# Kernel optimization log

Measured on AMD Instinct MI355X. Metric: run time of the kernel, lower is better.

## Reference

```python
import jax, jax.numpy as jnp
import numpy as np

N_ITER = 3


def squash(v):
    # v: [..., out_C]; scale by ||v||^2/(1+||v||^2) and normalize by ||v||
    sq = jnp.sum(v * v, axis=-1, keepdims=True)
    return (sq / (1.0 + sq)) * v / jnp.sqrt(sq)


def setup_inputs() -> dict:
    key = jax.random.key(0)
    k1, k2 = jax.random.split(key)
    B, n_nodes, n_caps, in_C, out_C = 64, 2048, 32, 16, 32
    x = jax.random.normal(k1, (B, n_nodes, in_C), dtype=jnp.float32)
    route_weights = 0.1 * jax.random.normal(k2, (n_nodes, n_caps, in_C, out_C), dtype=jnp.float32)
    return {"x": x, "route_weights": route_weights}


def reference(x, route_weights):
    # priors: [B, n_nodes, n_caps, out_C]
    priors = jnp.einsum('bni,nkio->bnko', x, route_weights)
    logits = jnp.zeros_like(priors)
    outputs = None
    for i in range(N_ITER):
        probs = jax.nn.softmax(logits, axis=2)            # over n_caps
        s = jnp.sum(probs * priors, axis=1, keepdims=True)  # [B,1,n_caps,out_C]
        outputs = squash(s)
        if i != N_ITER - 1:
            delta = jnp.sum(priors * outputs, axis=-1, keepdims=True)
            logits = logits + delta
    return outputs
```

## Files before the change

### kernel.cpp

```cpp
#include <hip/hip_runtime.h>
#include <math.h>


#define BATCH 64
#define NN    2048
#define NK    32
#define NI    16
#define NO    32

#define PNB   16
#define NSETS (NN / PNB)
#define XT_JS 528

typedef __bf16 bf16x8 __attribute__((ext_vector_type(8)));
typedef float  f32x16 __attribute__((ext_vector_type(16)));

__device__ __forceinline__ unsigned short f2bf(float f) {
    unsigned int x = __float_as_uint(f);
    unsigned int lsb = (x >> 16) & 1u;
    x += 0x7fffu + lsb;
    return (unsigned short)(x >> 16);
}
__device__ __forceinline__ float bflo(unsigned int u) { return __uint_as_float(u << 16); }
__device__ __forceinline__ float bfhi(unsigned int u) { return __uint_as_float(u & 0xffff0000u); }

__global__ __launch_bounds__(256) void wqt_kernel(const float* __restrict__ Wg,
                                                  unsigned short* __restrict__ wq) {
    const int w    = threadIdx.x >> 6;
    const int lane = threadIdx.x & 63;
    const int task = blockIdx.x * 4 + w;
    const int o  = lane & 31;
    const int ih = lane >> 5;
    const float* src = Wg + (size_t)task * (NI * NO);
    unsigned short d[8];
#pragma unroll
    for (int j = 0; j < 8; ++j)
        d[j] = f2bf(src[(ih * 8 + j) * NO + o]);
    *(uint4*)(wq + (size_t)task * (NO * NI) + o * NI + ih * 8) = *(uint4*)d;
}

template <int PASS>
__global__ __launch_bounds__(1024) void fused_pass(
    const float* __restrict__ xg,
    const unsigned short* __restrict__ wq,
    const float* __restrict__ outv,
    float* __restrict__ logits0,
    float* __restrict__ part)
{
    __shared__ unsigned short xt_lds[PNB * XT_JS];
    __shared__ float delta_lds[2][32 * 33];

    const int tid  = threadIdx.x;
    const int w    = tid >> 6;
    const int lane = tid & 63;
    const int l5   = lane & 31;
    const int h5   = lane >> 5;
    const int set  = blockIdx.x;
    const int hb   = blockIdx.y;
    const int k0   = 2 * w, k1 = 2 * w + 1;
    const int gb5  = hb * 32 + l5;
    const int sb   = tid >> 5;
    const int sk   = tid & 31;
    const int nbase = set * PNB;

#pragma unroll
    for (int rr = 0; rr < 2; ++rr) {
        const int id  = tid + rr * 1024;
        const int bl  = id >> 6;
        const int rem = id & 63;
        const int j   = rem >> 2;
        const int i4  = rem & 3;
        float4 v = *(const float4*)(xg + ((size_t)(hb * 32 + bl) * NN + (nbase + j)) * NI + i4 * 4);
        ushort4 o4;
        o4.x = f2bf(v.x); o4.y = f2bf(v.y); o4.z = f2bf(v.z); o4.w = f2bf(v.w);
        *(ushort4*)(xt_lds + j * XT_JS + bl * 16 + i4 * 4) = o4;
    }
    __syncthreads();

    unsigned orp0[8], orp1[8];
    if constexpr (PASS >= 1) {
#pragma unroll
        for (int q = 0; q < 8; ++q) {
            const int oA = ((2*q) & 3) + 8 * ((2*q) >> 2) + 4 * h5;
            const int oB = ((2*q+1) & 3) + 8 * ((2*q+1) >> 2) + 4 * h5;
            float a0 = outv[(k0 * NO + oA) * BATCH + gb5];
            float b0 = outv[(k0 * NO + oB) * BATCH + gb5];
            float a1 = outv[(k1 * NO + oA) * BATCH + gb5];
            float b1 = outv[(k1 * NO + oB) * BATCH + gb5];
            orp0[q] = (unsigned)f2bf(a0) | ((unsigned)f2bf(b0) << 16);
            orp1[q] = (unsigned)f2bf(a1) | ((unsigned)f2bf(b1) << 16);
        }
    }

    float sa0[16], sa1[16];
#pragma unroll
    for (int r = 0; r < 16; ++r) { sa0[r] = 0.f; sa1[r] = 0.f; }

    bf16x8 b0N, b1N;
    float gN = 0.f;
    {
        const int n = nbase;
        b0N = *(const bf16x8*)(wq + (size_t)n * (NK * NO * NI) + k0 * (NO * NI) + l5 * NI + h5 * 8);
        b1N = *(const bf16x8*)(wq + (size_t)n * (NK * NO * NI) + k1 * (NO * NI) + l5 * NI + h5 * 8);
        if constexpr (PASS == 2)
            gN = logits0[(size_t)n * (BATCH * NK) + hb * 1024 + tid];
    }

    int buf = 0;
    for (int j = 0; j < PNB; ++j) {
        const int n = nbase + j;
        const bf16x8 b0C = b0N, b1C = b1N;
        const float gC = gN;
        if (j < PNB - 1) {
            const int n2 = n + 1;
            b0N = *(const bf16x8*)(wq + (size_t)n2 * (NK * NO * NI) + k0 * (NO * NI) + l5 * NI + h5 * 8);
            b1N = *(const bf16x8*)(wq + (size_t)n2 * (NK * NO * NI) + k1 * (NO * NI) + l5 * NI + h5 * 8);
            if constexpr (PASS == 2)
                gN = logits0[(size_t)n2 * (BATCH * NK) + hb * 1024 + tid];
        }
        const bf16x8 aC = *(const bf16x8*)(xt_lds + j * XT_JS + l5 * 16 + h5 * 8);

        f32x16 c0, c1;
#pragma unroll
        for (int r = 0; r < 16; ++r) { c0[r] = 0.f; c1[r] = 0.f; }
        c0 = __builtin_amdgcn_mfma_f32_32x32x16_bf16(b0C, aC, c0, 0, 0, 0);
        c1 = __builtin_amdgcn_mfma_f32_32x32x16_bf16(b1C, aC, c1, 0, 0, 0);

        if constexpr (PASS == 0) {
#pragma unroll
            for (int r = 0; r < 16; ++r) { sa0[r] += c0[r]; sa1[r] += c1[r]; }
        } else {
            float d0 = 0.f, d1 = 0.f;
#pragma unroll
            for (int r = 0; r < 16; ++r) {
                const unsigned u0 = orp0[r >> 1], u1 = orp1[r >> 1];
                const float o0 = (r & 1) ? bfhi(u0) : bflo(u0);
                const float o1 = (r & 1) ? bfhi(u1) : bflo(u1);
                d0 = fmaf(c0[r], o0, d0);
                d1 = fmaf(c1[r], o1, d1);
            }
            d0 += __shfl_xor(d0, 32);
            d1 += __shfl_xor(d1, 32);

            delta_lds[buf][l5 * 33 + (h5 ? k1 : k0)] = h5 ? d1 : d0;
            __syncthreads();

            float l = delta_lds[buf][sb * 33 + sk];
            if constexpr (PASS == 1)
                logits0[(size_t)n * (BATCH * NK) + hb * 1024 + tid] = l;
            else
                l += gC;
            float e = __expf(l);
            float s = e;
#pragma unroll
            for (int mask = 1; mask < 32; mask <<= 1)
                s += __shfl_xor(s, mask);
            delta_lds[buf][sb * 33 + sk] = e / s;
            __syncthreads();

            const float p0 = delta_lds[buf][l5 * 33 + k0];
            const float p1 = delta_lds[buf][l5 * 33 + k1];
#pragma unroll
            for (int r = 0; r < 16; ++r) {
                sa0[r] = fmaf(p0, c0[r], sa0[r]);
                sa1[r] = fmaf(p1, c1[r], sa1[r]);
            }
            buf ^= 1;
        }
    }

    const float scale = (PASS == 0) ? (1.f / NK) : 1.f;
    float* pb = part + ((size_t)(hb * NSETS + set) << 15);
#pragma unroll
    for (int r = 0; r < 16; ++r) {
        const int o = (r & 3) + 8 * (r >> 2) + 4 * h5;
        pb[(k0 * NO + o) * 32 + l5] = sa0[r] * scale;
        pb[(k1 * NO + o) * 32 + l5] = sa1[r] * scale;
    }
}

template <int FINAL>
__global__ __launch_bounds__(1024) void reduce_squash3(
    const float* __restrict__ part,
    float* __restrict__ outv,
    float* __restrict__ outp)
{
    __shared__ float s_lds[32 * 33];
    __shared__ float cf_lds[32];
    const int k  = blockIdx.x;
    const int hb = blockIdx.y;
    const int t  = threadIdx.x;
    const int o  = t >> 5;
    const int b  = t & 31;

    const float* src = part + ((size_t)hb * NSETS << 15) + (k << 10) + (o << 5) + b;
    float v0 = 0.f, v1 = 0.f, v2 = 0.f, v3 = 0.f;
#pragma unroll 4
    for (int s = 0; s < NSETS; s += 4) {
        v0 += src[(size_t)(s + 0) << 15];
        v1 += src[(size_t)(s + 1) << 15];
        v2 += src[(size_t)(s + 2) << 15];
        v3 += src[(size_t)(s + 3) << 15];
    }
    const float v = (v0 + v1) + (v2 + v3);
    s_lds[o * 33 + b] = v;
    __syncthreads();
    if (t < 32) {
        float sq = 0.f;
#pragma unroll
        for (int oo = 0; oo < 32; ++oo) { const float x = s_lds[oo * 33 + t]; sq = fmaf(x, x, sq); }
        cf_lds[t] = sq / ((1.f + sq) * sqrtf(sq));
    }
    __syncthreads();
    if (FINAL) {
        const int bq = t >> 5, oq = t & 31;
        outp[(size_t)(hb * 32 + bq) * 1024 + k * 32 + oq] = s_lds[oq * 33 + bq] * cf_lds[bq];
    } else {
        outv[k * 2048 + o * 64 + hb * 32 + b] = v * cf_lds[b];
    }
}


#define LBB 32
#define LNCHUNK 8
#define LNBLK (NN / LNCHUNK)
#define LTHREADS 512
#define WK_STRIDE 516

template <int PASS>
__global__ __launch_bounds__(LTHREADS, 1) void legacy_pass(
    const float* __restrict__ xg, const float* __restrict__ Wg,
    const float* __restrict__ outvL, float* __restrict__ logits,
    float* __restrict__ partial)
{
    __shared__ float w_lds[NK * WK_STRIDE];
    __shared__ float x_lds[LBB][NI + 1];
    __shared__ float delta_lds[LBB][NK + 1];
    const int t = threadIdx.x, nb = blockIdx.x, bg = blockIdx.y;
    const int b0 = bg * LBB;
    const int k = t >> 4, bq = t & 15, bl0 = bq * 2, bl1 = bq * 2 + 1;
    float acc0[NO], acc1[NO];
#pragma unroll
    for (int o = 0; o < NO; ++o) { acc0[o] = 0.f; acc1[o] = 0.f; }
    float outr0[NO], outr1[NO];
    if constexpr (PASS >= 1) {
        const float4* o0 = (const float4*)&outvL[((b0 + bl0) * NK + k) * NO];
        const float4* o1 = (const float4*)&outvL[((b0 + bl1) * NK + k) * NO];
#pragma unroll
        for (int q = 0; q < NO / 4; ++q) {
            float4 a = o0[q]; float4 b = o1[q];
            outr0[4*q+0]=a.x; outr0[4*q+1]=a.y; outr0[4*q+2]=a.z; outr0[4*q+3]=a.w;
            outr1[4*q+0]=b.x; outr1[4*q+1]=b.y; outr1[4*q+2]=b.z; outr1[4*q+3]=b.w;
        }
    }
    for (int j = 0; j < LNCHUNK; ++j) {
        const int n = nb * LNCHUNK + j;
        __syncthreads();
        {
            const float4* src = (const float4*)(Wg + (size_t)n * (NK * NI * NO));
#pragma unroll
            for (int r = 0; r < (NK * NI * NO / 4) / LTHREADS; ++r) {
                int idx4 = t + r * LTHREADS;
                float4 v = src[idx4];
                int e = idx4 * 4, kk = e >> 9, rem = e & 511;
                *(float4*)&w_lds[kk * WK_STRIDE + rem] = v;
            }
        }
        { int bl = t >> 4, i = t & 15;
          x_lds[bl][i] = xg[((size_t)(b0 + bl) * NN + n) * NI + i]; }
        __syncthreads();
        if constexpr (PASS == 0) {
#pragma unroll
            for (int i = 0; i < NI; ++i) {
                float xa = x_lds[bl0][i], xb = x_lds[bl1][i];
                const float* wrow = &w_lds[k * WK_STRIDE + i * NO];
#pragma unroll
                for (int o = 0; o < NO; ++o) {
                    float w = wrow[o];
                    acc0[o] = fmaf(xa, w, acc0[o]);
                    acc1[o] = fmaf(xb, w, acc1[o]);
                }
            }
        } else {
            float pr0[NO], pr1[NO];
#pragma unroll
            for (int o = 0; o < NO; ++o) { pr0[o] = 0.f; pr1[o] = 0.f; }
#pragma unroll
            for (int i = 0; i < NI; ++i) {
                float xa = x_lds[bl0][i], xb = x_lds[bl1][i];
                const float* wrow = &w_lds[k * WK_STRIDE + i * NO];
#pragma unroll
                for (int o = 0; o < NO; ++o) {
                    float w = wrow[o];
                    pr0[o] = fmaf(xa, w, pr0[o]);
                    pr1[o] = fmaf(xb, w, pr1[o]);
                }
            }
            float d0 = 0.f, d1 = 0.f;
#pragma unroll
            for (int o = 0; o < NO; ++o) {
                d0 = fmaf(pr0[o], outr0[o], d0);
                d1 = fmaf(pr1[o], outr1[o], d1);
            }
            float l0 = d0, l1 = d1;
            const size_t li0 = ((size_t)(b0 + bl0) * NN + n) * NK + k;
            const size_t li1 = ((size_t)(b0 + bl1) * NN + n) * NK + k;
            if constexpr (PASS == 2) { l0 += logits[li0]; l1 += logits[li1]; }
            else { logits[li0] = d0; logits[li1] = d1; }
            delta_lds[bl0][k] = l0; delta_lds[bl1][k] = l1;
            __syncthreads();
            float m0 = -1e30f, m1 = -1e30f;
#pragma unroll
            for (int kk = 0; kk < NK; ++kk) {
                m0 = fmaxf(m0, delta_lds[bl0][kk]);
                m1 = fmaxf(m1, delta_lds[bl1][kk]);
            }
            float s0 = 0.f, s1 = 0.f;
#pragma unroll
            for (int kk = 0; kk < NK; ++kk) {
                s0 += __expf(delta_lds[bl0][kk] - m0);
                s1 += __expf(delta_lds[bl1][kk] - m1);
            }
            float p0 = __expf(l0 - m0) / s0;
            float p1 = __expf(l1 - m1) / s1;
#pragma unroll
            for (int o = 0; o < NO; ++o) {
                acc0[o] = fmaf(p0, pr0[o], acc0[o]);
                acc1[o] = fmaf(p1, pr1[o], acc1[o]);
            }
        }
    }
    const float scale = (PASS == 0) ? (1.f / NK) : 1.f;
    float4* p0 = (float4*)&partial[(((size_t)nb * BATCH + (b0 + bl0)) * NK + k) * NO];
    float4* p1 = (float4*)&partial[(((size_t)nb * BATCH + (b0 + bl1)) * NK + k) * NO];
#pragma unroll
    for (int q = 0; q < NO / 4; ++q) {
        float4 v0, v1;
        v0.x = acc0[4*q+0]*scale; v0.y = acc0[4*q+1]*scale;
        v0.z = acc0[4*q+2]*scale; v0.w = acc0[4*q+3]*scale;
        v1.x = acc1[4*q+0]*scale; v1.y = acc1[4*q+1]*scale;
        v1.z = acc1[4*q+2]*scale; v1.w = acc1[4*q+3]*scale;
        p0[q] = v0; p1[q] = v1;
    }
}

__global__ __launch_bounds__(256) void legacy_reduce(
    const float* __restrict__ partial, float* __restrict__ outf)
{
    const int tid = blockIdx.x * 256 + threadIdx.x;
    float v = 0.f;
    for (int nb = 0; nb < LNBLK; ++nb)
        v += partial[(size_t)nb * (BATCH * NK * NO) + tid];
    float sq = v * v;
#pragma unroll
    for (int off = 1; off < 32; off <<= 1) sq += __shfl_xor(sq, off);
    float coef = sq / ((1.f + sq) * sqrtf(sq));
    outf[tid] = v * coef;
}


extern "C" void kernel_launch(void* const* d_in, const int* in_sizes, int n_in,
                              void* d_out, int out_size, void* d_ws, size_t ws_size,
                              hipStream_t stream)
{
    const float* xg = (const float*)d_in[0];
    const float* Wg = (const float*)d_in[1];
    float* outp = (float*)d_out;
    char* ws = (char*)d_ws;

    const size_t SZ_WQ     = (size_t)NN * NK * NO * NI * 2;
    const size_t SZ_PART   = (size_t)256 * 32768 * 4;
    const size_t SZ_LOGITS = (size_t)NN * BATCH * NK * 4;
    const size_t SZ_OUTV   = (size_t)NK * NO * BATCH * 4;
    const size_t NEED = SZ_WQ + SZ_PART + SZ_LOGITS + SZ_OUTV;

    if (ws_size >= NEED) {
        unsigned short* wq = (unsigned short*)ws;
        float* part    = (float*)(ws + SZ_WQ);
        float* logits0 = (float*)(ws + SZ_WQ + SZ_PART);
        float* outv    = (float*)(ws + SZ_WQ + SZ_PART + SZ_LOGITS);

        wqt_kernel<<<16384, 256, 0, stream>>>(Wg, wq);

        dim3 pg(NSETS, 2);
        dim3 rg(NK, 2);
        fused_pass<0><<<pg, 1024, 0, stream>>>(xg, wq, nullptr, nullptr, part);
        reduce_squash3<0><<<rg, 1024, 0, stream>>>(part, outv, nullptr);
        fused_pass<1><<<pg, 1024, 0, stream>>>(xg, wq, outv, logits0, part);
        reduce_squash3<0><<<rg, 1024, 0, stream>>>(part, outv, nullptr);
        fused_pass<2><<<pg, 1024, 0, stream>>>(xg, wq, outv, logits0, part);
        reduce_squash3<1><<<rg, 1024, 0, stream>>>(part, nullptr, outp);
    } else {
        float* partial = (float*)ws;
        float* logits = (float*)(ws + (size_t)LNBLK * BATCH * NK * NO * 4);
        float* outvL = (float*)(ws + (size_t)LNBLK * BATCH * NK * NO * 4 + (size_t)BATCH * NN * NK * 4);
        dim3 grid(LNBLK, BATCH / LBB);
        const int rblocks = BATCH * NK * NO / 256;
        legacy_pass<0><<<grid, LTHREADS, 0, stream>>>(xg, Wg, nullptr, logits, partial);
        legacy_reduce<<<rblocks, 256, 0, stream>>>(partial, outvL);
        legacy_pass<1><<<grid, LTHREADS, 0, stream>>>(xg, Wg, outvL, logits, partial);
        legacy_reduce<<<rblocks, 256, 0, stream>>>(partial, outvL);
        legacy_pass<2><<<grid, LTHREADS, 0, stream>>>(xg, Wg, outvL, logits, partial);
        legacy_reduce<<<rblocks, 256, 0, stream>>>(partial, outp);
    }
}
```

Before: 334.0 us.

## Halve node sets per block and split reduction into chunked two-stage with fused squash

Cuts nodes per block from 16 to 8, which doubles the number of fused_pass blocks, and adds an occupancy hint to launch_bounds. The single 64-block reduction is split into a 4-way chunked stage1 reduction. The squash of the routing outputs is recomputed inside each fused_pass block from the partial sums, and a separate final kernel produces the output. The aim is to raise parallelism in both the main pass and the reduction, which previously had very few blocks. The cost is twice the partial-sum traffic, redundant squash work in every block, and one extra launch.

```diff
diff --git a/kernel.cpp b/kernel.cpp
--- a/kernel.cpp
+++ b/kernel.cpp
@@ -8,8 +8,9 @@
 #define NI    16
 #define NO    32
 
-#define PNB   16
+#define PNB   8
 #define NSETS (NN / PNB)
+#define NCH   4
 #define XT_JS 528
 
 typedef __bf16 bf16x8 __attribute__((ext_vector_type(8)));
@@ -40,10 +41,10 @@
 }
 
 template <int PASS>
-__global__ __launch_bounds__(1024) void fused_pass(
+__global__ __launch_bounds__(1024, 8) void fused_pass(
     const float* __restrict__ xg,
     const unsigned short* __restrict__ wq,
-    const float* __restrict__ outv,
+    const float* __restrict__ vpart,
     float* __restrict__ logits0,
     float* __restrict__ part)
 {
@@ -63,11 +64,9 @@
     const int sk   = tid & 31;
     const int nbase = set * PNB;
 
-#pragma unroll
-    for (int rr = 0; rr < 2; ++rr) {
-        const int id  = tid + rr * 1024;
-        const int bl  = id >> 6;
-        const int rem = id & 63;
+    {
+        const int bl  = tid >> 5;
+        const int rem = tid & 31;
         const int j   = rem >> 2;
         const int i4  = rem & 3;
         float4 v = *(const float4*)(xg + ((size_t)(hb * 32 + bl) * NN + (nbase + j)) * NI + i4 * 4);
@@ -79,16 +78,29 @@
 
     unsigned orp0[8], orp1[8];
     if constexpr (PASS >= 1) {
+        float v0[16], v1[16];
+        float sq0 = 0.f, sq1 = 0.f;
+#pragma unroll
+        for (int r = 0; r < 16; ++r) {
+            const int o = (r & 3) + 8 * (r >> 2) + 4 * h5;
+            float a = 0.f, b = 0.f;
+#pragma unroll
+            for (int c = 0; c < NCH; ++c) {
+                a += vpart[(((size_t)c * NK + k0) * NO + o) * BATCH + gb5];
+                b += vpart[(((size_t)c * NK + k1) * NO + o) * BATCH + gb5];
+            }
+            v0[r] = a; v1[r] = b;
+            sq0 = fmaf(a, a, sq0);
+            sq1 = fmaf(b, b, sq1);
+        }
+        sq0 += __shfl_xor(sq0, 32);
+        sq1 += __shfl_xor(sq1, 32);
+        const float cf0 = sq0 / ((1.f + sq0) * sqrtf(sq0));
+        const float cf1 = sq1 / ((1.f + sq1) * sqrtf(sq1));
 #pragma unroll
         for (int q = 0; q < 8; ++q) {
-            const int oA = ((2*q) & 3) + 8 * ((2*q) >> 2) + 4 * h5;
-            const int oB = ((2*q+1) & 3) + 8 * ((2*q+1) >> 2) + 4 * h5;
-            float a0 = outv[(k0 * NO + oA) * BATCH + gb5];
-            float b0 = outv[(k0 * NO + oB) * BATCH + gb5];
-            float a1 = outv[(k1 * NO + oA) * BATCH + gb5];
-            float b1 = outv[(k1 * NO + oB) * BATCH + gb5];
-            orp0[q] = (unsigned)f2bf(a0) | ((unsigned)f2bf(b0) << 16);
-            orp1[q] = (unsigned)f2bf(a1) | ((unsigned)f2bf(b1) << 16);
+            orp0[q] = (unsigned)f2bf(v0[2 * q] * cf0) | ((unsigned)f2bf(v0[2 * q + 1] * cf0) << 16);
+            orp1[q] = (unsigned)f2bf(v1[2 * q] * cf1) | ((unsigned)f2bf(v1[2 * q + 1] * cf1) << 16);
         }
     }
 
@@ -179,10 +191,32 @@
     }
 }
 
-template <int FINAL>
-__global__ __launch_bounds__(1024) void reduce_squash3(
+__global__ __launch_bounds__(1024) void reduce_stage1(
     const float* __restrict__ part,
-    float* __restrict__ outv,
+    float* __restrict__ vpart)
+{
+    const int k  = blockIdx.x;
+    const int hb = blockIdx.y;
+    const int c  = blockIdx.z;
+    const int t  = threadIdx.x;
+    const int o  = t >> 5;
+    const int b  = t & 31;
+
+    const float* src = part + ((size_t)(hb * NSETS + c * (NSETS / NCH)) << 15)
+                            + (k << 10) + (o << 5) + b;
+    float v0 = 0.f, v1 = 0.f, v2 = 0.f, v3 = 0.f;
+#pragma unroll 4
+    for (int s = 0; s < NSETS / NCH; s += 4) {
+        v0 += src[(size_t)(s + 0) << 15];
+        v1 += src[(size_t)(s + 1) << 15];
+        v2 += src[(size_t)(s + 2) << 15];
+        v3 += src[(size_t)(s + 3) << 15];
+    }
+    vpart[(((size_t)c * NK + k) * NO + o) * BATCH + hb * 32 + b] = (v0 + v1) + (v2 + v3);
+}
+
+__global__ __launch_bounds__(1024) void reduce_final(
+    const float* __restrict__ vpart,
     float* __restrict__ outp)
 {
     __shared__ float s_lds[32 * 33];
@@ -193,16 +227,10 @@
     const int o  = t >> 5;
     const int b  = t & 31;
 
-    const float* src = part + ((size_t)hb * NSETS << 15) + (k << 10) + (o << 5) + b;
-    float v0 = 0.f, v1 = 0.f, v2 = 0.f, v3 = 0.f;
-#pragma unroll 4
-    for (int s = 0; s < NSETS; s += 4) {
-        v0 += src[(size_t)(s + 0) << 15];
-        v1 += src[(size_t)(s + 1) << 15];
-        v2 += src[(size_t)(s + 2) << 15];
-        v3 += src[(size_t)(s + 3) << 15];
-    }
-    const float v = (v0 + v1) + (v2 + v3);
+    float v = 0.f;
+#pragma unroll
+    for (int c = 0; c < NCH; ++c)
+        v += vpart[(((size_t)c * NK + k) * NO + o) * BATCH + hb * 32 + b];
     s_lds[o * 33 + b] = v;
     __syncthreads();
     if (t < 32) {
@@ -212,12 +240,8 @@
         cf_lds[t] = sq / ((1.f + sq) * sqrtf(sq));
     }
     __syncthreads();
-    if (FINAL) {
-        const int bq = t >> 5, oq = t & 31;
-        outp[(size_t)(hb * 32 + bq) * 1024 + k * 32 + oq] = s_lds[oq * 33 + bq] * cf_lds[bq];
-    } else {
-        outv[k * 2048 + o * 64 + hb * 32 + b] = v * cf_lds[b];
-    }
+    const int bq = t >> 5, oq = t & 31;
+    outp[(size_t)(hb * 32 + bq) * 1024 + k * 32 + oq] = s_lds[oq * 33 + bq] * cf_lds[bq];
 }
 
 
@@ -369,27 +393,29 @@
     char* ws = (char*)d_ws;
 
     const size_t SZ_WQ     = (size_t)NN * NK * NO * NI * 2;
-    const size_t SZ_PART   = (size_t)256 * 32768 * 4;
+    const size_t SZ_PART   = (size_t)512 * 32768 * 4;
     const size_t SZ_LOGITS = (size_t)NN * BATCH * NK * 4;
-    const size_t SZ_OUTV   = (size_t)NK * NO * BATCH * 4;
-    const size_t NEED = SZ_WQ + SZ_PART + SZ_LOGITS + SZ_OUTV;
+    const size_t SZ_VPART  = (size_t)NCH * NK * NO * BATCH * 4;
+    const size_t NEED = SZ_WQ + SZ_PART + SZ_LOGITS + SZ_VPART;
 
     if (ws_size >= NEED) {
         unsigned short* wq = (unsigned short*)ws;
         float* part    = (float*)(ws + SZ_WQ);
         float* logits0 = (float*)(ws + SZ_WQ + SZ_PART);
-        float* outv    = (float*)(ws + SZ_WQ + SZ_PART + SZ_LOGITS);
+        float* vpart   = (float*)(ws + SZ_WQ + SZ_PART + SZ_LOGITS);
 
         wqt_kernel<<<16384, 256, 0, stream>>>(Wg, wq);
 
         dim3 pg(NSETS, 2);
-        dim3 rg(NK, 2);
+        dim3 rg(NK, 2, NCH);
+        dim3 fg(NK, 2);
         fused_pass<0><<<pg, 1024, 0, stream>>>(xg, wq, nullptr, nullptr, part);
-        reduce_squash3<0><<<rg, 1024, 0, stream>>>(part, outv, nullptr);
-        fused_pass<1><<<pg, 1024, 0, stream>>>(xg, wq, outv, logits0, part);
-        reduce_squash3<0><<<rg, 1024, 0, stream>>>(part, outv, nullptr);
-        fused_pass<2><<<pg, 1024, 0, stream>>>(xg, wq, outv, logits0, part);
-        reduce_squash3<1><<<rg, 1024, 0, stream>>>(part, nullptr, outp);
+        reduce_stage1<<<rg, 1024, 0, stream>>>(part, vpart);
+        fused_pass<1><<<pg, 1024, 0, stream>>>(xg, wq, vpart, logits0, part);
+        reduce_stage1<<<rg, 1024, 0, stream>>>(part, vpart);
+        fused_pass<2><<<pg, 1024, 0, stream>>>(xg, wq, vpart, logits0, part);
+        reduce_stage1<<<rg, 1024, 0, stream>>>(part, vpart);
+        reduce_final<<<fg, 1024, 0, stream>>>(vpart, outp);
     } else {
         float* partial = (float*)ws;
         float* logits = (float*)(ws + (size_t)LNBLK * BATCH * NK * NO * 4);
```

New measurement: 1.057 ms. 217% more time.
